# Kernel optimization log

Hardware: AMD Instinct MI355X
Metric: run time of the kernel (lower is better)

Reference implementation:

```python
import jax, jax.numpy as jnp
import numpy as np

B, T, C, H = 8, 2048, 1024, 16
D = C // H  # head dim


def setup_inputs() -> dict:
    key = jax.random.key(0)
    k1, k2, k3 = jax.random.split(key, 3)
    x = jax.random.normal(k1, (B, T, C), dtype=jnp.float32)
    attention_mask = jnp.ones((B, 1, T), dtype=jnp.int32)
    w_attn = jax.random.normal(k2, (C, 3 * C), dtype=jnp.float32) * 0.02
    b_attn = jnp.zeros((3 * C,), dtype=jnp.float32)
    w_proj = jax.random.normal(k3, (C, C), dtype=jnp.float32) * (0.02 / np.sqrt(2 * 12))
    b_proj = jnp.zeros((C,), dtype=jnp.float32)
    return {"x": x, "attention_mask": attention_mask, "w_attn": w_attn,
            "b_attn": b_attn, "w_proj": w_proj, "b_proj": b_proj}


def reference(x, attention_mask, w_attn, b_attn, w_proj, b_proj):
    Bx, Tx, Cx = x.shape
    qkv = x @ w_attn + b_attn                      # [B,T,3C]
    q, k, v = jnp.split(qkv, 3, axis=2)
    def heads(t):
        return t.reshape(Bx, Tx, H, D).transpose(0, 2, 1, 3)  # [B,H,T,D]
    q, k, v = heads(q), heads(k), heads(v)
    phi_q = jax.nn.elu(q) + 1.0
    phi_k = jax.nn.elu(k) + 1.0
    valid_keys = jnp.any(attention_mask > 0, axis=1).astype(x.dtype)  # [B,T]
    mask = valid_keys[:, None, :, None]            # [B,1,T,1]
    phi_k = phi_k * mask
    v = v * mask
    kv = jnp.einsum('bhtd,bhtf->bhdf', phi_k, v)   # [B,H,D,D]
    k_sum = jnp.sum(phi_k, axis=2, keepdims=True)  # [B,H,1,D]
    numerator = jnp.einsum('bhtd,bhdf->bhtf', phi_q, kv)       # [B,H,T,D]
    denominator = jnp.einsum('bhtd,bhrd->bhtr', phi_q, k_sum)  # [B,H,T,1]
    denominator = jnp.maximum(denominator, 1e-08)
    y = numerator / denominator
    y = y.transpose(0, 2, 1, 3).reshape(Bx, Tx, Cx)
    return y @ w_proj + b_proj
```

## Files before the change

### kernel.cpp

```cpp
#include <hip/hip_runtime.h>

#define Tdim 2048

typedef __attribute__((ext_vector_type(8))) short bf16x8;
typedef __attribute__((ext_vector_type(4))) float f32x4;
typedef __attribute__((ext_vector_type(4))) short short4v;

#define GLOBAL_U32(p) ((const __attribute__((address_space(1))) unsigned int*)(p))
#define LDS_U32(p)    ((__attribute__((address_space(3))) unsigned int*)(p))

__device__ __forceinline__ float phi_f(float x) {
    return x > 0.f ? (x + 1.f) : __expf(x);
}
__device__ __forceinline__ short f2bf(float f) {
    unsigned u = __float_as_uint(f);
    u += 0x7fffu + ((u >> 16) & 1u);
    return (short)(u >> 16);
}
__device__ __forceinline__ float bf2f(short h) {
    return __uint_as_float(((unsigned)(unsigned short)h) << 16);
}


__global__ __launch_bounds__(256) void split_tile_kernel(
    const float* __restrict__ X, short* __restrict__ Hi, short* __restrict__ Lo)
{
    const int rt = blockIdx.x;
    const int cb = blockIdx.y;
    const int t = threadIdx.x;
    const int rl = t >> 4;
    const int cc = t & 15;

    const float* xp = X + ((size_t)rt * 16 + rl) * 1024 + cb * 128 + cc * 8;
    const float4 a = *(const float4*)xp;
    const float4 b = *(const float4*)(xp + 4);
    float v[8] = {a.x, a.y, a.z, a.w, b.x, b.y, b.z, b.w};
    bf16x8 h, l;
#pragma unroll
    for (int j = 0; j < 8; ++j) {
        const short hh = f2bf(v[j]);
        h[j] = hh;
        l[j] = f2bf(v[j] - bf2f(hh));
    }
    const int kt = cb * 4 + (cc >> 2);
    const int slot = ((cc & 3) << 4) | rl;
    const size_t off = ((size_t)rt * 32 + kt) * 512 + slot * 8;
    *(bf16x8*)(Hi + off) = h;
    *(bf16x8*)(Lo + off) = l;
}

__global__ __launch_bounds__(256) void w_tile_kernel(
    const float* __restrict__ W, int N,
    short* __restrict__ Thi, short* __restrict__ Tlo)
{
    const int tile = blockIdx.x * 4 + (threadIdx.x >> 6);
    const int nt = tile >> 5;
    const int kt = tile & 31;
    const int lane = threadIdx.x & 63;
    const int n = nt * 16 + (lane & 15);
    const int k = kt * 32 + (lane >> 4) * 8;
    const float* wp = W + (size_t)k * N + n;
    bf16x8 h, l;
#pragma unroll
    for (int j = 0; j < 8; ++j) {
        const float v = wp[(size_t)j * N];
        const short hh = f2bf(v);
        h[j] = hh;
        l[j] = f2bf(v - bf2f(hh));
    }
    const size_t off = (size_t)tile * 512 + lane * 8;
    *(bf16x8*)(Thi + off) = h;
    *(bf16x8*)(Tlo + off) = l;
}

template<int AMODE>
__global__ __launch_bounds__(512, 2) void gemm3_kernel(
    const short* __restrict__ Ahi, const short* __restrict__ Alo, int lda,
    const short* __restrict__ BThi, const short* __restrict__ BTlo,
    const float* __restrict__ bias, float* __restrict__ C,
    int K, int ldc)
{
    __shared__ short smem[65536];
    const int tid = threadIdx.x;
    const int lane = tid & 63;
    const int wid = tid >> 6;
    const int bx = blockIdx.x, by = blockIdx.y;
    const int wm = wid >> 2, wn = wid & 3;

    const size_t tilestep = (size_t)(K >> 5) * 512;

    const int sel = wid >> 1, half = wid & 1;
    const short* gptr;
    if (sel >= 2) {
        const short* gb = (sel == 2) ? BThi : BTlo;
        gptr = gb + (size_t)(bx * 16 + half * 8) * tilestep + lane * 8;
    } else if (AMODE == 0) {
        const short* gb = (sel == 0) ? Ahi : Alo;
        gptr = gb + (size_t)(by * 16 + half * 8) * tilestep + lane * 8;
    } else {
        const short* gb = Ahi;
        gptr = gb + ((size_t)by * 256 + half * 128 + (lane & 15)) * (size_t)lda
                  + (lane >> 4) * 8 + (sel == 1 ? 64 : 0);
    }
    short* lw = smem + sel * 8192 + half * 4096;

    f32x4 acc[8][4];
#pragma unroll
    for (int i = 0; i < 8; ++i)
#pragma unroll
        for (int j = 0; j < 4; ++j) acc[i][j] = (f32x4){0.f, 0.f, 0.f, 0.f};

    auto stage = [&](int buf, int k0) {
        short* lb = lw + buf * 32768;
        if (AMODE == 0 || sel >= 2) {
            const short* g = gptr + (size_t)(k0 >> 5) * 512;
#pragma unroll
            for (int c = 0; c < 8; ++c)
                __builtin_amdgcn_global_load_lds(
                    GLOBAL_U32(g + (size_t)c * tilestep),
                    LDS_U32(lb + c * 512), 16, 0, 0);
        } else {
            const int koff = ((k0 >> 6) << 7) + (k0 & 63);
            const short* g = gptr + koff;
#pragma unroll
            for (int c = 0; c < 8; ++c)
                __builtin_amdgcn_global_load_lds(
                    GLOBAL_U32(g + (size_t)(c * 16) * lda),
                    LDS_U32(lb + c * 512), 16, 0, 0);
        }
    };

    stage(0, 0);
    __syncthreads();

    const int fo = lane * 8;
    int cur = 0;
    for (int k0 = 0; k0 < K; k0 += 32) {
        if (k0 + 32 < K) stage(cur ^ 1, k0 + 32);

        const short* bp = smem + cur * 32768;
        bf16x8 bh[4], bl[4];
#pragma unroll
        for (int j = 0; j < 4; ++j) {
            bh[j] = *(const bf16x8*)(bp + 16384 + (wn * 4 + j) * 512 + fo);
            bl[j] = *(const bf16x8*)(bp + 24576 + (wn * 4 + j) * 512 + fo);
        }
        __builtin_amdgcn_s_setprio(1);
#pragma unroll
        for (int i = 0; i < 8; ++i) {
            const bf16x8 ah = *(const bf16x8*)(bp + (wm * 8 + i) * 512 + fo);
            const bf16x8 al = *(const bf16x8*)(bp + 8192 + (wm * 8 + i) * 512 + fo);
#pragma unroll
            for (int j = 0; j < 4; ++j) {
                acc[i][j] = __builtin_amdgcn_mfma_f32_16x16x32_bf16(ah, bh[j], acc[i][j], 0, 0, 0);
                acc[i][j] = __builtin_amdgcn_mfma_f32_16x16x32_bf16(al, bh[j], acc[i][j], 0, 0, 0);
                acc[i][j] = __builtin_amdgcn_mfma_f32_16x16x32_bf16(ah, bl[j], acc[i][j], 0, 0, 0);
            }
        }
        __builtin_amdgcn_s_setprio(0);
        __syncthreads();
        cur ^= 1;
    }

    const int fr = lane & 15, fq = lane >> 4;
#pragma unroll
    for (int i = 0; i < 8; ++i) {
        const size_t row0 = (size_t)by * 256 + wm * 128 + i * 16 + fq * 4;
#pragma unroll
        for (int j = 0; j < 4; ++j) {
            const int col = bx * 256 + wn * 64 + j * 16 + fr;
            const float bv = bias[col];
            float* cp = C + row0 * (size_t)ldc + col;
#pragma unroll
            for (int r = 0; r < 4; ++r)
                cp[(size_t)r * ldc] = acc[i][j][r] + bv;
        }
    }
}

__global__ __launch_bounds__(256) void kv_part_kernel(
    const float* __restrict__ qkv, const int* __restrict__ attn,
    float* __restrict__ kvpart, float* __restrict__ kspart)
{
    __shared__ float ks[32][64];
    __shared__ float vs[32][64];

    const int chunk = blockIdx.x;
    const int bh = blockIdx.y;
    const int b = bh >> 4;
    const int h = bh & 15;
    const int tid = threadIdx.x;
    const int tx = tid & 15;
    const int ty = tid >> 4;
    const int l_t = tid >> 4;
    const int l_d = (tid & 15) << 2;

    const float* kb = qkv + (size_t)b * Tdim * 3072 + 1024 + h * 64;
    const float* vb = qkv + (size_t)b * Tdim * 3072 + 2048 + h * 64;
    const int* am = attn + b * Tdim;

    float acc[4][4];
#pragma unroll
    for (int i = 0; i < 4; ++i)
#pragma unroll
        for (int j = 0; j < 4; ++j) acc[i][j] = 0.f;
    float ksl = 0.f;

    for (int t0 = chunk * 256; t0 < (chunk + 1) * 256; t0 += 32) {
        __syncthreads();
#pragma unroll
        for (int rr = 0; rr < 2; ++rr) {
            const int t = l_t + rr * 16;
            const int gt = t0 + t;
            const float m = (am[gt] > 0) ? 1.f : 0.f;
            const float4 k4 = *(const float4*)(kb + (size_t)gt * 3072 + l_d);
            const float4 v4 = *(const float4*)(vb + (size_t)gt * 3072 + l_d);
            float4 kp, vp;
            kp.x = phi_f(k4.x) * m; kp.y = phi_f(k4.y) * m;
            kp.z = phi_f(k4.z) * m; kp.w = phi_f(k4.w) * m;
            vp.x = v4.x * m; vp.y = v4.y * m; vp.z = v4.z * m; vp.w = v4.w * m;
            *(float4*)&ks[t][l_d] = kp;
            *(float4*)&vs[t][l_d] = vp;
        }
        __syncthreads();
#pragma unroll
        for (int t = 0; t < 32; ++t) {
            float kr[4], vr[4];
            *(float4*)kr = *(const float4*)&ks[t][ty * 4];
            *(float4*)vr = *(const float4*)&vs[t][tx * 4];
#pragma unroll
            for (int i = 0; i < 4; ++i)
#pragma unroll
                for (int j = 0; j < 4; ++j)
                    acc[i][j] = fmaf(kr[i], vr[j], acc[i][j]);
        }
        if (tid < 64) {
#pragma unroll
            for (int t = 0; t < 32; ++t) ksl += ks[t][tid];
        }
    }

    float* ko = kvpart + ((size_t)bh * 8 + chunk) * 4096;
#pragma unroll
    for (int i = 0; i < 4; ++i) {
        float4 o;
        o.x = acc[i][0]; o.y = acc[i][1]; o.z = acc[i][2]; o.w = acc[i][3];
        *(float4*)(ko + (ty * 4 + i) * 64 + tx * 4) = o;
    }
    if (tid < 64) kspart[((size_t)bh * 8 + chunk) * 64 + tid] = ksl;
}

__global__ __launch_bounds__(256) void kv_reduce_kernel(
    const float* __restrict__ kvpart, const float* __restrict__ kspart,
    float* __restrict__ kv, float* __restrict__ ksum)
{
    const int bh = blockIdx.x;
    const int tid = threadIdx.x;
    const float4* p = (const float4*)(kvpart + (size_t)bh * 8 * 4096);
    float4 s0 = {0,0,0,0}, s1 = {0,0,0,0}, s2 = {0,0,0,0}, s3 = {0,0,0,0};
#pragma unroll
    for (int c = 0; c < 8; ++c) {
        const int base = c * 1024;
        float4 a = p[base + tid], b = p[base + 256 + tid],
               cc = p[base + 512 + tid], d = p[base + 768 + tid];
        s0.x += a.x; s0.y += a.y; s0.z += a.z; s0.w += a.w;
        s1.x += b.x; s1.y += b.y; s1.z += b.z; s1.w += b.w;
        s2.x += cc.x; s2.y += cc.y; s2.z += cc.z; s2.w += cc.w;
        s3.x += d.x; s3.y += d.y; s3.z += d.z; s3.w += d.w;
    }
    float4* o = (float4*)(kv + (size_t)bh * 4096);
    o[tid] = s0; o[256 + tid] = s1; o[512 + tid] = s2; o[768 + tid] = s3;
    if (tid < 64) {
        float ss = 0.f;
#pragma unroll
        for (int c = 0; c < 8; ++c) ss += kspart[((size_t)bh * 8 + c) * 64 + tid];
        ksum[bh * 64 + tid] = ss;
    }
}

__global__ __launch_bounds__(256) void attn_y_kernel(
    float* __restrict__ qkv, const float* __restrict__ kvin,
    const float* __restrict__ ksumin)
{
    __shared__ float qs[64][65];
    __shared__ float kvs[64][64];
    __shared__ float dinv[64];
    __shared__ float ksums[64];

    const int bh = blockIdx.y;
    const int b = bh >> 4;
    const int hh = bh & 15;
    const int t0 = blockIdx.x * 64;
    const int tid = threadIdx.x;
    const int tx = tid & 15;
    const int ty = tid >> 4;

    const float4* kvg = (const float4*)(kvin + (size_t)bh * 4096);
#pragma unroll
    for (int i = 0; i < 4; ++i)
        ((float4*)kvs)[tid + i * 256] = kvg[tid + i * 256];
    if (tid < 64) ksums[tid] = ksumin[bh * 64 + tid];

    float* qb = qkv + ((size_t)(b * Tdim + t0)) * 3072 + hh * 64;
#pragma unroll
    for (int rr = 0; rr < 4; ++rr) {
        const int t = (tid >> 4) + rr * 16;
        const int dd = (tid & 15) << 2;
        const float4 q4 = *(const float4*)(qb + (size_t)t * 3072 + dd);
        qs[t][dd + 0] = phi_f(q4.x);
        qs[t][dd + 1] = phi_f(q4.y);
        qs[t][dd + 2] = phi_f(q4.z);
        qs[t][dd + 3] = phi_f(q4.w);
    }
    __syncthreads();

    if (tid < 64) {
        float s = 0.f;
#pragma unroll
        for (int d = 0; d < 64; ++d) s = fmaf(qs[tid][d], ksums[d], s);
        dinv[tid] = 1.f / fmaxf(s, 1e-8f);
    }
    __syncthreads();

    float acc[4][4];
#pragma unroll
    for (int i = 0; i < 4; ++i)
#pragma unroll
        for (int j = 0; j < 4; ++j) acc[i][j] = 0.f;

#pragma unroll 4
    for (int d = 0; d < 64; ++d) {
        float qr[4];
        qr[0] = qs[ty * 4 + 0][d];
        qr[1] = qs[ty * 4 + 1][d];
        qr[2] = qs[ty * 4 + 2][d];
        qr[3] = qs[ty * 4 + 3][d];
        const float4 kr = *(const float4*)&kvs[d][tx * 4];
#pragma unroll
        for (int i = 0; i < 4; ++i) {
            acc[i][0] = fmaf(qr[i], kr.x, acc[i][0]);
            acc[i][1] = fmaf(qr[i], kr.y, acc[i][1]);
            acc[i][2] = fmaf(qr[i], kr.z, acc[i][2]);
            acc[i][3] = fmaf(qr[i], kr.w, acc[i][3]);
        }
    }

    short* qout = (short*)qkv + ((size_t)(b * Tdim + t0)) * 6144 + hh * 128;
#pragma unroll
    for (int i = 0; i < 4; ++i) {
        const float di = dinv[ty * 4 + i];
        short4v hv, lv;
#pragma unroll
        for (int j = 0; j < 4; ++j) {
            const float val = acc[i][j] * di;
            const short h = f2bf(val);
            hv[j] = h;
            lv[j] = f2bf(val - bf2f(h));
        }
        short* rp = qout + (size_t)(ty * 4 + i) * 6144;
        *(short4v*)(rp + tx * 4) = hv;
        *(short4v*)(rp + 64 + tx * 4) = lv;
    }
}

extern "C" void kernel_launch(void* const* d_in, const int* in_sizes, int n_in,
                              void* d_out, int out_size, void* d_ws, size_t ws_size,
                              hipStream_t stream)
{
    const float* x      = (const float*)d_in[0];
    const int*   attn   = (const int*)  d_in[1];
    const float* w_attn = (const float*)d_in[2];
    const float* b_attn = (const float*)d_in[3];
    const float* w_proj = (const float*)d_in[4];
    const float* b_proj = (const float*)d_in[5];
    float* out = (float*)d_out;

    char* ws = (char*)d_ws;
    size_t off = 0;
    auto alloc = [&](size_t bytes) { void* p = ws + off; off = (off + bytes + 255) & ~(size_t)255; return p; };
    float* qkv   = (float*)alloc((size_t)16384 * 3072 * 4);
    short* waThi = (short*)alloc((size_t)3072 * 1024 * 2);
    short* waTlo = (short*)alloc((size_t)3072 * 1024 * 2);
    short* wpThi = (short*)alloc((size_t)1024 * 1024 * 2);
    short* wpTlo = (short*)alloc((size_t)1024 * 1024 * 2);
    float* kvb   = (float*)alloc((size_t)128 * 4096 * 4);
    float* ksum  = (float*)alloc((size_t)128 * 64 * 4);

    short* xhi = (short*)d_out;
    short* xlo = xhi + (size_t)16384 * 1024;
    float* kvpart = (float*)d_out;
    float* kspart = (float*)((char*)d_out + (size_t)128 * 8 * 4096 * 4);

    split_tile_kernel<<<dim3(1024, 8), 256, 0, stream>>>(x, xhi, xlo);
    w_tile_kernel<<<1536, 256, 0, stream>>>(w_attn, 3072, waThi, waTlo);
    w_tile_kernel<<<512, 256, 0, stream>>>(w_proj, 1024, wpThi, wpTlo);
    gemm3_kernel<0><<<dim3(12, 64), 512, 0, stream>>>(xhi, xlo, 0, waThi, waTlo, b_attn, qkv, 1024, 3072);
    kv_part_kernel<<<dim3(8, 128), 256, 0, stream>>>(qkv, attn, kvpart, kspart);
    kv_reduce_kernel<<<128, 256, 0, stream>>>(kvpart, kspart, kvb, ksum);
    attn_y_kernel<<<dim3(32, 128), 256, 0, stream>>>(qkv, kvb, ksum);
    gemm3_kernel<1><<<dim3(4, 64), 512, 0, stream>>>((const short*)qkv, (const short*)qkv, 6144,
                                                     wpThi, wpTlo, b_proj, out, 1024, 1024);
}
```

Baseline: 593.0 us.

## Interleave split prefetch and LDS fragment loads with MFMA phases in GEMM loop

```diff
diff --git a/kernel.cpp b/kernel.cpp
--- a/kernel.cpp
+++ b/kernel.cpp
@@ -8,6 +8,14 @@
 
 #define GLOBAL_U32(p) ((const __attribute__((address_space(1))) unsigned int*)(p))
 #define LDS_U32(p)    ((__attribute__((address_space(3))) unsigned int*)(p))
+
+#define WAIT_LGKM0() do { asm volatile("s_waitcnt lgkmcnt(0)" ::: "memory"); \
+                          __builtin_amdgcn_sched_barrier(0); } while (0)
+#define WAIT_VM0()   do { asm volatile("s_waitcnt vmcnt(0)" ::: "memory"); \
+                          __builtin_amdgcn_sched_barrier(0); } while (0)
+#define BAR()        do { __builtin_amdgcn_sched_barrier(0); \
+                          __builtin_amdgcn_s_barrier(); \
+                          __builtin_amdgcn_sched_barrier(0); } while (0)
 
 __device__ __forceinline__ float phi_f(float x) {
     return x > 0.f ? (x + 1.f) : __expf(x);
@@ -110,12 +118,12 @@
 #pragma unroll
         for (int j = 0; j < 4; ++j) acc[i][j] = (f32x4){0.f, 0.f, 0.f, 0.f};
 
-    auto stage = [&](int buf, int k0) {
+    auto stage4 = [&](int buf, int k0, int part) {
         short* lb = lw + buf * 32768;
         if (AMODE == 0 || sel >= 2) {
             const short* g = gptr + (size_t)(k0 >> 5) * 512;
 #pragma unroll
-            for (int c = 0; c < 8; ++c)
+            for (int c = part * 4; c < part * 4 + 4; ++c)
                 __builtin_amdgcn_global_load_lds(
                     GLOBAL_U32(g + (size_t)c * tilestep),
                     LDS_U32(lb + c * 512), 16, 0, 0);
@@ -123,42 +131,79 @@
             const int koff = ((k0 >> 6) << 7) + (k0 & 63);
             const short* g = gptr + koff;
 #pragma unroll
-            for (int c = 0; c < 8; ++c)
+            for (int c = part * 4; c < part * 4 + 4; ++c)
                 __builtin_amdgcn_global_load_lds(
                     GLOBAL_U32(g + (size_t)(c * 16) * lda),
                     LDS_U32(lb + c * 512), 16, 0, 0);
         }
     };
 
-    stage(0, 0);
-    __syncthreads();
+    stage4(0, 0, 0);
+    stage4(0, 0, 1);
+    WAIT_VM0();
+    BAR();
 
     const int fo = lane * 8;
     int cur = 0;
     for (int k0 = 0; k0 < K; k0 += 32) {
-        if (k0 + 32 < K) stage(cur ^ 1, k0 + 32);
-
         const short* bp = smem + cur * 32768;
+        const short* ab = bp + wm * 8 * 512;
+        const bool pf = (k0 + 32 < K);
+
         bf16x8 bh[4], bl[4];
+        bf16x8 ah0, al0, ah1, al1;
+
+        auto lda2 = [&](int i0) {
+            ah0 = *(const bf16x8*)(ab + i0 * 512 + fo);
+            al0 = *(const bf16x8*)(ab + 8192 + i0 * 512 + fo);
+            ah1 = *(const bf16x8*)(ab + (i0 + 1) * 512 + fo);
+            al1 = *(const bf16x8*)(ab + 8192 + (i0 + 1) * 512 + fo);
+        };
+        auto mm2 = [&](int base) {
+            __builtin_amdgcn_s_setprio(1);
+#pragma unroll
+            for (int j = 0; j < 4; ++j) {
+                acc[base][j]     = __builtin_amdgcn_mfma_f32_16x16x32_bf16(ah0, bh[j], acc[base][j], 0, 0, 0);
+                acc[base][j]     = __builtin_amdgcn_mfma_f32_16x16x32_bf16(al0, bh[j], acc[base][j], 0, 0, 0);
+                acc[base][j]     = __builtin_amdgcn_mfma_f32_16x16x32_bf16(ah0, bl[j], acc[base][j], 0, 0, 0);
+                acc[base + 1][j] = __builtin_amdgcn_mfma_f32_16x16x32_bf16(ah1, bh[j], acc[base + 1][j], 0, 0, 0);
+                acc[base + 1][j] = __builtin_amdgcn_mfma_f32_16x16x32_bf16(al1, bh[j], acc[base + 1][j], 0, 0, 0);
+                acc[base + 1][j] = __builtin_amdgcn_mfma_f32_16x16x32_bf16(ah1, bl[j], acc[base + 1][j], 0, 0, 0);
+            }
+            __builtin_amdgcn_s_setprio(0);
+        };
+
+        if (pf) stage4(cur ^ 1, k0 + 32, 0);
 #pragma unroll
         for (int j = 0; j < 4; ++j) {
             bh[j] = *(const bf16x8*)(bp + 16384 + (wn * 4 + j) * 512 + fo);
             bl[j] = *(const bf16x8*)(bp + 24576 + (wn * 4 + j) * 512 + fo);
         }
-        __builtin_amdgcn_s_setprio(1);
-#pragma unroll
-        for (int i = 0; i < 8; ++i) {
-            const bf16x8 ah = *(const bf16x8*)(bp + (wm * 8 + i) * 512 + fo);
-            const bf16x8 al = *(const bf16x8*)(bp + 8192 + (wm * 8 + i) * 512 + fo);
-#pragma unroll
-            for (int j = 0; j < 4; ++j) {
-                acc[i][j] = __builtin_amdgcn_mfma_f32_16x16x32_bf16(ah, bh[j], acc[i][j], 0, 0, 0);
-                acc[i][j] = __builtin_amdgcn_mfma_f32_16x16x32_bf16(al, bh[j], acc[i][j], 0, 0, 0);
-                acc[i][j] = __builtin_amdgcn_mfma_f32_16x16x32_bf16(ah, bl[j], acc[i][j], 0, 0, 0);
-            }
-        }
-        __builtin_amdgcn_s_setprio(0);
-        __syncthreads();
+        lda2(0);
+        BAR();
+        WAIT_LGKM0();
+        mm2(0);
+        BAR();
+
+        if (pf) stage4(cur ^ 1, k0 + 32, 1);
+        lda2(2);
+        BAR();
+        WAIT_LGKM0();
+        mm2(2);
+        BAR();
+
+        lda2(4);
+        BAR();
+        WAIT_LGKM0();
+        mm2(4);
+        BAR();
+
+        lda2(6);
+        BAR();
+        WAIT_LGKM0();
+        mm2(6);
+        WAIT_VM0();
+        BAR();
         cur ^= 1;
     }
 
```

Result: no change. 594.9 us (+0.3%).
